# Kernel optimization log

Hardware: AMD Instinct MI355X
Metric: run time of the kernel (lower is better)

## Reference

```python
import jax, jax.numpy as jnp
import numpy as np

N = 20000
E = 640000
D = 128


def setup_inputs() -> dict:
    key = jax.random.key(0)
    ks = jax.random.split(key, 8)
    x = jax.random.normal(ks[0], (N, D), dtype=jnp.float32)
    edge_index = jax.random.randint(ks[1], (2, E), 0, N, dtype=jnp.int64)
    s = 1.0 / np.sqrt(D)
    inp = {"x": x, "edge_index": edge_index}
    for i, layer in enumerate([2, 4, 6]):
        inp[f"W{i+1}"] = jax.random.uniform(ks[layer], (D, D), jnp.float32, -s, s)
        inp[f"b{i+1}"] = jax.random.uniform(ks[layer + 1], (D,), jnp.float32, -s, s)
    return inp


def _gcn_layer(x, src, dst, deg_inv, W, b):
    # linear (torch convention: y = x @ W.T + b), W: [out, in]
    xt = x @ W.T + b
    # gather source-node features, scatter-mean onto targets
    msg = xt[src]                                   # [E, D]
    agg = jax.ops.segment_sum(msg, dst, num_segments=N)  # [N, D]
    agg = agg * deg_inv[:, None]                    # mean over incoming edges
    return jax.nn.relu(agg) + xt


def reference(x, edge_index, W1, b1, W2, b2, W3, b3):
    src, dst = edge_index[0], edge_index[1]
    deg = jax.ops.segment_sum(jnp.ones((E,), jnp.float32), dst, num_segments=N)
    deg_inv = jnp.where(deg > 0, 1.0 / jnp.maximum(deg, 1.0), 0.0)
    for W, b in ((W1, b1), (W2, b2), (W3, b3)):
        x = _gcn_layer(x, src, dst, deg_inv, W, b)
    return x
```

## Files before the change

kernel.cpp:

```cpp
#include <hip/hip_runtime.h>

#define DD 128
#define KC 32
#define MT 64
#define ELLC 128
#define ELLI 124
#define NBMAX 320
#define ACAP 2304
#define AEPW 4096
#define AGGB 2048

__device__ __forceinline__ unsigned f2bf_rne(float f) {
    unsigned u = __float_as_uint(f);
    u += 0x7fffu + ((u >> 16) & 1u);
    return u >> 16;
}

__device__ __forceinline__ void gemm_body(float (*Xs)[MT + 4], float (*Ws)[DD + 4],
                                          const float* x,
                                          const float* __restrict__ W,
                                          const float* __restrict__ b,
                                          float* xt,
                                          unsigned* __restrict__ xtb, int M, int PS, int blk) {
    const int tid  = threadIdx.x;
    const int cg_  = tid & 15;
    const int rg   = tid >> 4;
    const int row0 = blk * MT;

    float acc[4][8];
#pragma unroll
    for (int i = 0; i < 4; ++i)
#pragma unroll
        for (int j = 0; j < 8; ++j) acc[i][j] = 0.0f;

    for (int kc = 0; kc < DD; kc += KC) {
#pragma unroll
        for (int it = 0; it < 2; ++it) {
            int idx = tid + it * 256;
            int r = idx >> 3, kq = idx & 7;
            int gr = row0 + r;
            float4 v = make_float4(0.f, 0.f, 0.f, 0.f);
            if (gr < M) v = *(const float4*)&x[gr * DD + kc + kq * 4];
            Xs[kq * 4 + 0][r] = v.x; Xs[kq * 4 + 1][r] = v.y;
            Xs[kq * 4 + 2][r] = v.z; Xs[kq * 4 + 3][r] = v.w;
        }
#pragma unroll
        for (int it = 0; it < 4; ++it) {
            int idx = tid + it * 256;
            int o = idx >> 3, kq = idx & 7;
            float4 v = *(const float4*)&W[o * DD + kc + kq * 4];
            Ws[kq * 4 + 0][o] = v.x; Ws[kq * 4 + 1][o] = v.y;
            Ws[kq * 4 + 2][o] = v.z; Ws[kq * 4 + 3][o] = v.w;
        }
        __syncthreads();

#pragma unroll 8
        for (int k = 0; k < KC; ++k) {
            float4 xv = *(const float4*)&Xs[k][rg * 4];
            float4 w0 = *(const float4*)&Ws[k][cg_ * 8];
            float4 w1 = *(const float4*)&Ws[k][cg_ * 8 + 4];
            float xr[4] = {xv.x, xv.y, xv.z, xv.w};
            float wc[8] = {w0.x, w0.y, w0.z, w0.w, w1.x, w1.y, w1.z, w1.w};
#pragma unroll
            for (int i = 0; i < 4; ++i)
#pragma unroll
                for (int j = 0; j < 8; ++j) acc[i][j] += xr[i] * wc[j];
        }
        __syncthreads();
    }

    float4 b0 = *(const float4*)&b[cg_ * 8];
    float4 b1 = *(const float4*)&b[cg_ * 8 + 4];
    float bb[8] = {b0.x, b0.y, b0.z, b0.w, b1.x, b1.y, b1.z, b1.w};
#pragma unroll
    for (int i = 0; i < 4; ++i) {
        int gr = row0 + rg * 4 + i;
        if (gr < M) {
            float v[8];
#pragma unroll
            for (int j = 0; j < 8; ++j) v[j] = acc[i][j] + bb[j];
            *(float4*)&xt[gr * DD + cg_ * 8]     = make_float4(v[0], v[1], v[2], v[3]);
            *(float4*)&xt[gr * DD + cg_ * 8 + 4] = make_float4(v[4], v[5], v[6], v[7]);
            uint4 p;
            p.x = f2bf_rne(v[0]) | (f2bf_rne(v[1]) << 16);
            p.y = f2bf_rne(v[2]) | (f2bf_rne(v[3]) << 16);
            p.z = f2bf_rne(v[4]) | (f2bf_rne(v[5]) << 16);
            p.w = f2bf_rne(v[6]) | (f2bf_rne(v[7]) << 16);
            unsigned* xp = xtb + (size_t)(cg_ >> 3) * ((size_t)PS * 32)
                               + (size_t)gr * 32 + ((cg_ & 7) << 2);
            *(uint4*)xp = p;
        }
    }
}

__global__ __launch_bounds__(256) void gemm_xwT(const float* x,
                                                const float* __restrict__ W,
                                                const float* __restrict__ b,
                                                float* xt,
                                                unsigned* __restrict__ xtb, int M, int PS) {
    __shared__ float Xs[KC][MT + 4];
    __shared__ float Ws[KC][DD + 4];
    gemm_body(Xs, Ws, x, W, b, xt, xtb, M, PS, blockIdx.x);
}

__global__ __launch_bounds__(256) void gemm1_plus_binA(const float* x,
                                                       const float* __restrict__ W,
                                                       const float* __restrict__ b,
                                                       float* xt,
                                                       unsigned* __restrict__ xtb, int M, int PS,
                                                       const int* __restrict__ src,
                                                       const int* __restrict__ dst,
                                                       int* __restrict__ bucket_count,
                                                       unsigned* __restrict__ bstore,
                                                       int E, int NB, int PA) {
    __shared__ float Xs[KC][MT + 4];
    __shared__ float Ws[KC][DD + 4];
    __shared__ int hist[NBMAX];
    __shared__ int basec[NBMAX];
    __shared__ int cur[NBMAX];

    if ((int)blockIdx.x >= PA) {
        gemm_body(Xs, Ws, x, W, b, xt, xtb, M, PS, blockIdx.x - PA);
        return;
    }

    const int tid = threadIdx.x;
    for (int i = tid; i < NB; i += 256) hist[i] = 0;
    __syncthreads();

    int dv[16], sv[16];
    const int ebase = blockIdx.x * AEPW;
#pragma unroll
    for (int r = 0; r < 4; ++r) {
        int e = ebase + r * 1024 + tid * 4;
        if (e + 4 <= E) {
            int4 d4 = *(const int4*)&dst[e];
            int4 s4 = *(const int4*)&src[e];
            dv[r*4+0] = d4.x; dv[r*4+1] = d4.y; dv[r*4+2] = d4.z; dv[r*4+3] = d4.w;
            sv[r*4+0] = s4.x; sv[r*4+1] = s4.y; sv[r*4+2] = s4.z; sv[r*4+3] = s4.w;
        } else {
#pragma unroll
            for (int q = 0; q < 4; ++q) {
                int ee = e + q;
                if (ee < E) { dv[r*4+q] = dst[ee]; sv[r*4+q] = src[ee]; }
                else        { dv[r*4+q] = -1;      sv[r*4+q] = 0; }
            }
        }
    }
#pragma unroll
    for (int i = 0; i < 16; ++i)
        if (dv[i] >= 0) atomicAdd(&hist[dv[i] >> 6], 1);
    __syncthreads();

    for (int bk = tid; bk < NB; bk += 256) {
        int h = hist[bk];
        basec[bk] = h ? atomicAdd(&bucket_count[bk], h) : 0;
        cur[bk] = 0;
    }
    __syncthreads();

#pragma unroll
    for (int i = 0; i < 16; ++i) {
        if (dv[i] >= 0) {
            int bk = dv[i] >> 6;
            int pos = basec[bk] + atomicAdd(&cur[bk], 1);
            if (pos < ACAP)
                bstore[bk * ACAP + pos] = ((unsigned)(dv[i] & 63) << 16) | (unsigned)sv[i];
        }
    }
}

__global__ __launch_bounds__(256) void ell_build(const unsigned* __restrict__ bstore,
                                                 const int* __restrict__ bucket_count,
                                                 unsigned short* __restrict__ colell,
                                                 unsigned* __restrict__ xtb,
                                                 int PS, int N) {
    __shared__ int c64[64];
    const int bk = blockIdx.x;
    for (int i = threadIdx.x; i < 64; i += 256) c64[i] = 0;
    __syncthreads();
    int cnt = bucket_count[bk];
    if (cnt > ACAP) cnt = ACAP;
    for (int i = threadIdx.x; i < cnt; i += 256) {
        unsigned code = bstore[bk * ACAP + i];
        int local = (int)(code >> 16);
        int s     = (int)(code & 0xffffu);
        int p = atomicAdd(&c64[local], 1);
        if (p < ELLI)
            colell[((((bk << 6) + local)) << 7) + p] = (unsigned short)s;
    }
    __syncthreads();
    if (threadIdx.x < 64) {
        int node = (bk << 6) + threadIdx.x;
        if (node < N) {
            int d = c64[threadIdx.x];
            int stored = d < ELLI ? d : ELLI;
            int padded = (stored + 3) & ~3;
            unsigned short* row = colell + ((size_t)node << 7);
            for (int p2 = stored; p2 < padded; ++p2) row[p2] = (unsigned short)N;
            row[127] = (unsigned short)(d < 65535 ? d : 65535);
        }
    }
    if (bk == 0 && threadIdx.x >= 64 && threadIdx.x < 80) {
        int i  = threadIdx.x - 64;
        int pl = i >> 3;
        int j  = i & 7;
        *(uint4*)&xtb[((size_t)pl * PS + (size_t)N) * 32 + (size_t)j * 4] =
            make_uint4(0u, 0u, 0u, 0u);
    }
}

__global__ __launch_bounds__(256, 8) void gcn_aggregate(const uint2* __restrict__ xtb2,
                                                        const float* xt,
                                                        const unsigned* __restrict__ colell32,
                                                        float* out, int PS, int N) {
    const int lane = threadIdx.x & 63;
    const int wid  = (int)blockIdx.x * 4 + (threadIdx.x >> 6);
    const int NW   = (int)gridDim.x * 4;
    const int T    = 2 * N;
    if (wid >= T) return;
    const int h = lane & 15;
    const int q = lane >> 4;

    int t = wid;
    int node0 = (t >= N) ? t - N : t;
    unsigned pk = colell32[((size_t)node0 << 6) + lane];

    while (t < T) {
        const int tn    = t + NW;
        const int node  = (t >= N) ? t - N : t;
        const int plane = (t >= N) ? 1 : 0;
        const uint2* __restrict__ xl = xtb2 + (size_t)plane * ((size_t)PS << 4) + h;

        const unsigned w63 = __shfl(pk, 63, 64);
        const int cnt = (int)(w63 >> 16);
        const int cl  = cnt < ELLI ? cnt : ELLI;
        const int cq  = (cl + 3) >> 2;

        float4 t4 = make_float4(0.f, 0.f, 0.f, 0.f);
        if (q == 0)
            t4 = ((const float4*)xt)[(size_t)node * 32 + plane * 16 + h];

        float a0 = 0.f, a1 = 0.f, a2 = 0.f, a3 = 0.f;
        unsigned pkn = 0;
        bool first = true;

        int tq = 0;
        while (tq < cq) {
            int f = cq - tq; if (f > 8) f = 8;
            uint2 u[8];
#pragma unroll
            for (int j = 0; j < 8; ++j) if (j < f) {
                int e = ((tq + j) << 2) | q;
                unsigned w = __shfl(pk, e >> 1, 64);
                int s = (e & 1) ? (int)(w >> 16) : (int)(w & 0xffffu);
                u[j] = xl[(size_t)s << 4];
            }
            if (first) {
                if (tn < T) {
                    int nnode = (tn >= N) ? tn - N : tn;
                    pkn = colell32[((size_t)nnode << 6) + lane];
                }
                first = false;
            }
#pragma unroll
            for (int j = 0; j < 8; ++j) if (j < f) {
                a0 += __uint_as_float(u[j].x << 16);
                a1 += __uint_as_float(u[j].x & 0xffff0000u);
                a2 += __uint_as_float(u[j].y << 16);
                a3 += __uint_as_float(u[j].y & 0xffff0000u);
            }
            tq += f;
        }
        if (first && tn < T) {
            int nnode = (tn >= N) ? tn - N : tn;
            pkn = colell32[((size_t)nnode << 6) + lane];
        }

        a0 += __shfl_down(a0, 32, 64); a1 += __shfl_down(a1, 32, 64);
        a2 += __shfl_down(a2, 32, 64); a3 += __shfl_down(a3, 32, 64);
        a0 += __shfl_down(a0, 16, 64); a1 += __shfl_down(a1, 16, 64);
        a2 += __shfl_down(a2, 16, 64); a3 += __shfl_down(a3, 16, 64);

        if (q == 0) {
            const float di = (cnt > 0) ? (1.0f / (float)cnt) : 0.0f;
            float4 o;
            o.x = fmaxf(a0 * di, 0.f) + t4.x;
            o.y = fmaxf(a1 * di, 0.f) + t4.y;
            o.z = fmaxf(a2 * di, 0.f) + t4.z;
            o.w = fmaxf(a3 * di, 0.f) + t4.w;
            ((float4*)out)[(size_t)node * 32 + plane * 16 + h] = o;
        }

        t = tn;
        pk = pkn;
    }
}

extern "C" void kernel_launch(void* const* d_in, const int* in_sizes, int n_in,
                              void* d_out, int out_size, void* d_ws, size_t ws_size,
                              hipStream_t stream) {
    const float* x  = (const float*)d_in[0];
    const int*   ei = (const int*)d_in[1];
    const float* W1 = (const float*)d_in[2];
    const float* b1 = (const float*)d_in[3];
    const float* W2 = (const float*)d_in[4];
    const float* b2 = (const float*)d_in[5];
    const float* W3 = (const float*)d_in[6];
    const float* b3 = (const float*)d_in[7];

    const int N  = in_sizes[0] / DD;
    const int E  = in_sizes[1] / 2;
    const int PS = N + 1;

    const int* src = ei;
    const int* dst = ei + E;

    const int NB = (N + 63) >> 6;
    const int PA = (E + AEPW - 1) / AEPW;
    const int GB = (N + MT - 1) / MT;

    char* ws = (char*)d_ws;
    size_t off = 0;
    auto alloc = [&](size_t bytes) {
        void* p = ws + off;
        off += (bytes + 255) & ~(size_t)255;
        return p;
    };
    int*            bucket_count = (int*)alloc((size_t)NB * sizeof(int));
    unsigned*       bstore       = (unsigned*)alloc((size_t)NB * ACAP * sizeof(unsigned));
    unsigned short* colell       = (unsigned short*)alloc((size_t)NB * 64 * ELLC * sizeof(unsigned short));
    unsigned*       xtb          = (unsigned*)alloc((size_t)PS * 256);

    float* xbuf = (float*)d_out;

    hipMemsetAsync(bucket_count, 0, (size_t)NB * sizeof(int), stream);
    gemm1_plus_binA<<<PA + GB, 256, 0, stream>>>(x, W1, b1, xbuf, xtb, N, PS,
                                                 src, dst, bucket_count, bstore, E, NB, PA);
    ell_build<<<NB, 256, 0, stream>>>(bstore, bucket_count, colell, xtb, PS, N);

    gcn_aggregate<<<AGGB, 256, 0, stream>>>((const uint2*)xtb, xbuf,
                                            (const unsigned*)colell, xbuf, PS, N);

    gemm_xwT<<<GB, 256, 0, stream>>>(xbuf, W2, b2, xbuf, xtb, N, PS);
    gcn_aggregate<<<AGGB, 256, 0, stream>>>((const uint2*)xtb, xbuf,
                                            (const unsigned*)colell, xbuf, PS, N);

    gemm_xwT<<<GB, 256, 0, stream>>>(xbuf, W3, b3, xbuf, xtb, N, PS);
    gcn_aggregate<<<AGGB, 256, 0, stream>>>((const uint2*)xtb, xbuf,
                                            (const unsigned*)colell, xbuf, PS, N);
}
```

Before: 208.8 us.

## Use split-bf16 MFMA for node linear transforms with precomputed weight splits

```diff
diff --git a/kernel.cpp b/kernel.cpp
--- a/kernel.cpp
+++ b/kernel.cpp
@@ -1,7 +1,6 @@
 #include <hip/hip_runtime.h>
 
 #define DD 128
-#define KC 32
 #define MT 64
 #define ELLC 128
 #define ELLI 124
@@ -10,117 +9,143 @@
 #define AEPW 4096
 #define AGGB 2048
 
+typedef __attribute__((ext_vector_type(8))) short bf16x8;
+typedef __attribute__((ext_vector_type(4))) float f32x4;
+
 __device__ __forceinline__ unsigned f2bf_rne(float f) {
     unsigned u = __float_as_uint(f);
     u += 0x7fffu + ((u >> 16) & 1u);
     return u >> 16;
 }
 
-__device__ __forceinline__ void gemm_body(float (*Xs)[MT + 4], float (*Ws)[DD + 4],
-                                          const float* x,
-                                          const float* __restrict__ W,
-                                          const float* __restrict__ b,
-                                          float* xt,
-                                          unsigned* __restrict__ xtb, int M, int PS, int blk) {
-    const int tid  = threadIdx.x;
-    const int cg_  = tid & 15;
-    const int rg   = tid >> 4;
-    const int row0 = blk * MT;
-
-    float acc[4][8];
-#pragma unroll
-    for (int i = 0; i < 4; ++i)
-#pragma unroll
-        for (int j = 0; j < 8; ++j) acc[i][j] = 0.0f;
-
-    for (int kc = 0; kc < DD; kc += KC) {
-#pragma unroll
-        for (int it = 0; it < 2; ++it) {
-            int idx = tid + it * 256;
-            int r = idx >> 3, kq = idx & 7;
-            int gr = row0 + r;
-            float4 v = make_float4(0.f, 0.f, 0.f, 0.f);
-            if (gr < M) v = *(const float4*)&x[gr * DD + kc + kq * 4];
-            Xs[kq * 4 + 0][r] = v.x; Xs[kq * 4 + 1][r] = v.y;
-            Xs[kq * 4 + 2][r] = v.z; Xs[kq * 4 + 3][r] = v.w;
-        }
-#pragma unroll
-        for (int it = 0; it < 4; ++it) {
-            int idx = tid + it * 256;
-            int o = idx >> 3, kq = idx & 7;
-            float4 v = *(const float4*)&W[o * DD + kc + kq * 4];
-            Ws[kq * 4 + 0][o] = v.x; Ws[kq * 4 + 1][o] = v.y;
-            Ws[kq * 4 + 2][o] = v.z; Ws[kq * 4 + 3][o] = v.w;
-        }
-        __syncthreads();
-
-#pragma unroll 8
-        for (int k = 0; k < KC; ++k) {
-            float4 xv = *(const float4*)&Xs[k][rg * 4];
-            float4 w0 = *(const float4*)&Ws[k][cg_ * 8];
-            float4 w1 = *(const float4*)&Ws[k][cg_ * 8 + 4];
-            float xr[4] = {xv.x, xv.y, xv.z, xv.w};
-            float wc[8] = {w0.x, w0.y, w0.z, w0.w, w1.x, w1.y, w1.z, w1.w};
-#pragma unroll
-            for (int i = 0; i < 4; ++i)
-#pragma unroll
-                for (int j = 0; j < 8; ++j) acc[i][j] += xr[i] * wc[j];
-        }
-        __syncthreads();
-    }
-
-    float4 b0 = *(const float4*)&b[cg_ * 8];
-    float4 b1 = *(const float4*)&b[cg_ * 8 + 4];
-    float bb[8] = {b0.x, b0.y, b0.z, b0.w, b1.x, b1.y, b1.z, b1.w};
-#pragma unroll
-    for (int i = 0; i < 4; ++i) {
-        int gr = row0 + rg * 4 + i;
+__device__ __forceinline__ bf16x8 pack8(const unsigned h[8]) {
+    union { uint4 u; bf16x8 v; } t;
+    t.u.x = h[0] | (h[1] << 16);
+    t.u.y = h[2] | (h[3] << 16);
+    t.u.z = h[4] | (h[5] << 16);
+    t.u.w = h[6] | (h[7] << 16);
+    return t.v;
+}
+
+__global__ __launch_bounds__(256) void prep(const float* __restrict__ W1,
+                                            const float* __restrict__ W2,
+                                            const float* __restrict__ W3,
+                                            unsigned short* __restrict__ whi,
+                                            unsigned short* __restrict__ wlo,
+                                            int* __restrict__ bucket_count, int NB) {
+    const int bk = blockIdx.x;
+    if (bk < 3) {
+        const float* W = (bk == 0) ? W1 : (bk == 1 ? W2 : W3);
+        unsigned short* h = whi + bk * (DD * DD);
+        unsigned short* l = wlo + bk * (DD * DD);
+        for (int i = threadIdx.x; i < DD * DD; i += 256) {
+            float x = W[i];
+            unsigned uh = f2bf_rne(x);
+            float fh = __uint_as_float(uh << 16);
+            h[i] = (unsigned short)uh;
+            l[i] = (unsigned short)f2bf_rne(x - fh);
+        }
+    } else {
+        for (int i = threadIdx.x; i < NB; i += 256) bucket_count[i] = 0;
+    }
+}
+
+__device__ __forceinline__ void gemm_body_mfma(const float* x,
+                                               const unsigned short* __restrict__ whi,
+                                               const unsigned short* __restrict__ wlo,
+                                               const float* __restrict__ b,
+                                               float* xt,
+                                               unsigned short* __restrict__ xtb16,
+                                               int M, int PS, int blk) {
+    const int lane = threadIdx.x & 63;
+    const int wv   = threadIdx.x >> 6;
+    const int r0   = blk * MT + wv * 16;
+    const int m    = lane & 15;
+    const int kg   = lane >> 4;
+    const int gr   = r0 + m;
+
+    f32x4 acc[8];
+#pragma unroll
+    for (int c = 0; c < 8; ++c) acc[c] = (f32x4){0.f, 0.f, 0.f, 0.f};
+
+#pragma unroll
+    for (int ks = 0; ks < 4; ++ks) {
+        const int kb = ks * 32 + kg * 8;
+        float4 v0 = make_float4(0.f, 0.f, 0.f, 0.f), v1 = v0;
         if (gr < M) {
-            float v[8];
-#pragma unroll
-            for (int j = 0; j < 8; ++j) v[j] = acc[i][j] + bb[j];
-            *(float4*)&xt[gr * DD + cg_ * 8]     = make_float4(v[0], v[1], v[2], v[3]);
-            *(float4*)&xt[gr * DD + cg_ * 8 + 4] = make_float4(v[4], v[5], v[6], v[7]);
-            uint4 p;
-            p.x = f2bf_rne(v[0]) | (f2bf_rne(v[1]) << 16);
-            p.y = f2bf_rne(v[2]) | (f2bf_rne(v[3]) << 16);
-            p.z = f2bf_rne(v[4]) | (f2bf_rne(v[5]) << 16);
-            p.w = f2bf_rne(v[6]) | (f2bf_rne(v[7]) << 16);
-            unsigned* xp = xtb + (size_t)(cg_ >> 3) * ((size_t)PS * 32)
-                               + (size_t)gr * 32 + ((cg_ & 7) << 2);
-            *(uint4*)xp = p;
+            v0 = *(const float4*)&x[(size_t)gr * DD + kb];
+            v1 = *(const float4*)&x[(size_t)gr * DD + kb + 4];
+        }
+        float xv[8] = {v0.x, v0.y, v0.z, v0.w, v1.x, v1.y, v1.z, v1.w};
+        unsigned hh[8], ll[8];
+#pragma unroll
+        for (int j = 0; j < 8; ++j) {
+            unsigned uh = f2bf_rne(xv[j]);
+            float fh = __uint_as_float(uh << 16);
+            hh[j] = uh;
+            ll[j] = f2bf_rne(xv[j] - fh);
+        }
+        bf16x8 ah = pack8(hh), al = pack8(ll);
+
+#pragma unroll
+        for (int c = 0; c < 8; ++c) {
+            const int ncol = c * 16 + m;
+            union { uint4 u; bf16x8 v; } bh, bl;
+            bh.u = *(const uint4*)&whi[(size_t)ncol * DD + kb];
+            bl.u = *(const uint4*)&wlo[(size_t)ncol * DD + kb];
+            acc[c] = __builtin_amdgcn_mfma_f32_16x16x32_bf16(ah, bh.v, acc[c], 0, 0, 0);
+            acc[c] = __builtin_amdgcn_mfma_f32_16x16x32_bf16(ah, bl.v, acc[c], 0, 0, 0);
+            acc[c] = __builtin_amdgcn_mfma_f32_16x16x32_bf16(al, bh.v, acc[c], 0, 0, 0);
+        }
+    }
+
+    const int rbase = r0 + kg * 4;
+#pragma unroll
+    for (int c = 0; c < 8; ++c) {
+        const int ncol  = c * 16 + m;
+        const float bias = b[ncol];
+        const int plane = ncol >> 6;
+        const int c64   = ncol & 63;
+#pragma unroll
+        for (int rg = 0; rg < 4; ++rg) {
+            const int grr = rbase + rg;
+            if (grr < M) {
+                float v = acc[c][rg] + bias;
+                xt[(size_t)grr * DD + ncol] = v;
+                xtb16[((size_t)plane * PS + grr) * 64 + c64] = (unsigned short)f2bf_rne(v);
+            }
         }
     }
 }
 
 __global__ __launch_bounds__(256) void gemm_xwT(const float* x,
-                                                const float* __restrict__ W,
+                                                const unsigned short* __restrict__ whi,
+                                                const unsigned short* __restrict__ wlo,
                                                 const float* __restrict__ b,
                                                 float* xt,
-                                                unsigned* __restrict__ xtb, int M, int PS) {
-    __shared__ float Xs[KC][MT + 4];
-    __shared__ float Ws[KC][DD + 4];
-    gemm_body(Xs, Ws, x, W, b, xt, xtb, M, PS, blockIdx.x);
+                                                unsigned short* __restrict__ xtb16,
+                                                int M, int PS) {
+    gemm_body_mfma(x, whi, wlo, b, xt, xtb16, M, PS, blockIdx.x);
 }
 
 __global__ __launch_bounds__(256) void gemm1_plus_binA(const float* x,
-                                                       const float* __restrict__ W,
+                                                       const unsigned short* __restrict__ whi,
+                                                       const unsigned short* __restrict__ wlo,
                                                        const float* __restrict__ b,
                                                        float* xt,
-                                                       unsigned* __restrict__ xtb, int M, int PS,
+                                                       unsigned short* __restrict__ xtb16,
+                                                       int M, int PS,
                                                        const int* __restrict__ src,
                                                        const int* __restrict__ dst,
                                                        int* __restrict__ bucket_count,
                                                        unsigned* __restrict__ bstore,
                                                        int E, int NB, int PA) {
-    __shared__ float Xs[KC][MT + 4];
-    __shared__ float Ws[KC][DD + 4];
     __shared__ int hist[NBMAX];
     __shared__ int basec[NBMAX];
     __shared__ int cur[NBMAX];
 
     if ((int)blockIdx.x >= PA) {
-        gemm_body(Xs, Ws, x, W, b, xt, xtb, M, PS, blockIdx.x - PA);
+        gemm_body_mfma(x, whi, wlo, b, xt, xtb16, M, PS, blockIdx.x - PA);
         return;
     }
 
@@ -331,22 +356,28 @@
     unsigned*       bstore       = (unsigned*)alloc((size_t)NB * ACAP * sizeof(unsigned));
     unsigned short* colell       = (unsigned short*)alloc((size_t)NB * 64 * ELLC * sizeof(unsigned short));
     unsigned*       xtb          = (unsigned*)alloc((size_t)PS * 256);
+    unsigned short* whi          = (unsigned short*)alloc((size_t)3 * DD * DD * sizeof(unsigned short));
+    unsigned short* wlo          = (unsigned short*)alloc((size_t)3 * DD * DD * sizeof(unsigned short));
 
     float* xbuf = (float*)d_out;
-
-    hipMemsetAsync(bucket_count, 0, (size_t)NB * sizeof(int), stream);
-    gemm1_plus_binA<<<PA + GB, 256, 0, stream>>>(x, W1, b1, xbuf, xtb, N, PS,
+    unsigned short* xtb16 = (unsigned short*)xtb;
+
+    prep<<<4, 256, 0, stream>>>(W1, W2, W3, whi, wlo, bucket_count, NB);
+
+    gemm1_plus_binA<<<PA + GB, 256, 0, stream>>>(x, whi, wlo, b1, xbuf, xtb16, N, PS,
                                                  src, dst, bucket_count, bstore, E, NB, PA);
     ell_build<<<NB, 256, 0, stream>>>(bstore, bucket_count, colell, xtb, PS, N);
 
     gcn_aggregate<<<AGGB, 256, 0, stream>>>((const uint2*)xtb, xbuf,
                                             (const unsigned*)colell, xbuf, PS, N);
 
-    gemm_xwT<<<GB, 256, 0, stream>>>(xbuf, W2, b2, xbuf, xtb, N, PS);
+    gemm_xwT<<<GB, 256, 0, stream>>>(xbuf, whi + DD * DD, wlo + DD * DD, b2,
+                                     xbuf, xtb16, N, PS);
     gcn_aggregate<<<AGGB, 256, 0, stream>>>((const uint2*)xtb, xbuf,
                                             (const unsigned*)colell, xbuf, PS, N);
 
-    gemm_xwT<<<GB, 256, 0, stream>>>(xbuf, W3, b3, xbuf, xtb, N, PS);
+    gemm_xwT<<<GB, 256, 0, stream>>>(xbuf, whi + 2 * DD * DD, wlo + 2 * DD * DD, b3,
+                                     xbuf, xtb16, N, PS);
     gcn_aggregate<<<AGGB, 256, 0, stream>>>((const uint2*)xtb, xbuf,
                                             (const unsigned*)colell, xbuf, PS, N);
 }
```

After: 226.0 us. 1.08x slower.

## Build ELL adjacency by direct per-node atomic scatter instead of bucketed two-pass

Applied to the files above, without the earlier changes.

```diff
diff --git a/kernel.cpp b/kernel.cpp
--- a/kernel.cpp
+++ b/kernel.cpp
@@ -5,8 +5,6 @@
 #define MT 64
 #define ELLC 128
 #define ELLI 124
-#define NBMAX 320
-#define ACAP 2304
 #define AEPW 4096
 #define AGGB 2048
 
@@ -103,31 +101,25 @@
     gemm_body(Xs, Ws, x, W, b, xt, xtb, M, PS, blockIdx.x);
 }
 
-__global__ __launch_bounds__(256) void gemm1_plus_binA(const float* x,
+__global__ __launch_bounds__(256) void gemm1_plus_scat(const float* x,
                                                        const float* __restrict__ W,
                                                        const float* __restrict__ b,
                                                        float* xt,
                                                        unsigned* __restrict__ xtb, int M, int PS,
                                                        const int* __restrict__ src,
                                                        const int* __restrict__ dst,
-                                                       int* __restrict__ bucket_count,
-                                                       unsigned* __restrict__ bstore,
-                                                       int E, int NB, int PA) {
+                                                       int* __restrict__ deg,
+                                                       unsigned short* __restrict__ colell,
+                                                       int E, int SB) {
     __shared__ float Xs[KC][MT + 4];
     __shared__ float Ws[KC][DD + 4];
-    __shared__ int hist[NBMAX];
-    __shared__ int basec[NBMAX];
-    __shared__ int cur[NBMAX];
-
-    if ((int)blockIdx.x >= PA) {
-        gemm_body(Xs, Ws, x, W, b, xt, xtb, M, PS, blockIdx.x - PA);
+
+    if ((int)blockIdx.x >= SB) {
+        gemm_body(Xs, Ws, x, W, b, xt, xtb, M, PS, blockIdx.x - SB);
         return;
     }
 
     const int tid = threadIdx.x;
-    for (int i = tid; i < NB; i += 256) hist[i] = 0;
-    __syncthreads();
-
     int dv[16], sv[16];
     const int ebase = blockIdx.x * AEPW;
 #pragma unroll
@@ -148,61 +140,30 @@
         }
     }
 #pragma unroll
-    for (int i = 0; i < 16; ++i)
-        if (dv[i] >= 0) atomicAdd(&hist[dv[i] >> 6], 1);
-    __syncthreads();
-
-    for (int bk = tid; bk < NB; bk += 256) {
-        int h = hist[bk];
-        basec[bk] = h ? atomicAdd(&bucket_count[bk], h) : 0;
-        cur[bk] = 0;
-    }
-    __syncthreads();
-
-#pragma unroll
     for (int i = 0; i < 16; ++i) {
         if (dv[i] >= 0) {
-            int bk = dv[i] >> 6;
-            int pos = basec[bk] + atomicAdd(&cur[bk], 1);
-            if (pos < ACAP)
-                bstore[bk * ACAP + pos] = ((unsigned)(dv[i] & 63) << 16) | (unsigned)sv[i];
-        }
-    }
-}
-
-__global__ __launch_bounds__(256) void ell_build(const unsigned* __restrict__ bstore,
-                                                 const int* __restrict__ bucket_count,
-                                                 unsigned short* __restrict__ colell,
-                                                 unsigned* __restrict__ xtb,
-                                                 int PS, int N) {
-    __shared__ int c64[64];
-    const int bk = blockIdx.x;
-    for (int i = threadIdx.x; i < 64; i += 256) c64[i] = 0;
-    __syncthreads();
-    int cnt = bucket_count[bk];
-    if (cnt > ACAP) cnt = ACAP;
-    for (int i = threadIdx.x; i < cnt; i += 256) {
-        unsigned code = bstore[bk * ACAP + i];
-        int local = (int)(code >> 16);
-        int s     = (int)(code & 0xffffu);
-        int p = atomicAdd(&c64[local], 1);
-        if (p < ELLI)
-            colell[((((bk << 6) + local)) << 7) + p] = (unsigned short)s;
-    }
-    __syncthreads();
-    if (threadIdx.x < 64) {
-        int node = (bk << 6) + threadIdx.x;
-        if (node < N) {
-            int d = c64[threadIdx.x];
-            int stored = d < ELLI ? d : ELLI;
-            int padded = (stored + 3) & ~3;
-            unsigned short* row = colell + ((size_t)node << 7);
-            for (int p2 = stored; p2 < padded; ++p2) row[p2] = (unsigned short)N;
-            row[127] = (unsigned short)(d < 65535 ? d : 65535);
-        }
-    }
-    if (bk == 0 && threadIdx.x >= 64 && threadIdx.x < 80) {
-        int i  = threadIdx.x - 64;
+            int pos = atomicAdd(&deg[dv[i]], 1);
+            if (pos < ELLI)
+                colell[((size_t)dv[i] << 7) + pos] = (unsigned short)sv[i];
+        }
+    }
+}
+
+__global__ __launch_bounds__(256) void ell_pad(unsigned short* __restrict__ colell,
+                                               const int* __restrict__ deg,
+                                               unsigned* __restrict__ xtb,
+                                               int PS, int N) {
+    const int node = (int)blockIdx.x * 256 + threadIdx.x;
+    if (node < N) {
+        int d = deg[node];
+        int stored = d < ELLI ? d : ELLI;
+        int padded = (stored + 3) & ~3;
+        unsigned short* row = colell + ((size_t)node << 7);
+        for (int p2 = stored; p2 < padded; ++p2) row[p2] = (unsigned short)N;
+        row[127] = (unsigned short)(d < 65535 ? d : 65535);
+    }
+    if (blockIdx.x == 0 && threadIdx.x < 16) {
+        int i  = threadIdx.x;
         int pl = i >> 3;
         int j  = i & 7;
         *(uint4*)&xtb[((size_t)pl * PS + (size_t)N) * 32 + (size_t)j * 4] =
@@ -316,9 +277,9 @@
     const int* src = ei;
     const int* dst = ei + E;
 
-    const int NB = (N + 63) >> 6;
-    const int PA = (E + AEPW - 1) / AEPW;
+    const int SB = (E + AEPW - 1) / AEPW;
     const int GB = (N + MT - 1) / MT;
+    const int PB = (N + 255) / 256;
 
     char* ws = (char*)d_ws;
     size_t off = 0;
@@ -327,17 +288,16 @@
         off += (bytes + 255) & ~(size_t)255;
         return p;
     };
-    int*            bucket_count = (int*)alloc((size_t)NB * sizeof(int));
-    unsigned*       bstore       = (unsigned*)alloc((size_t)NB * ACAP * sizeof(unsigned));
-    unsigned short* colell       = (unsigned short*)alloc((size_t)NB * 64 * ELLC * sizeof(unsigned short));
-    unsigned*       xtb          = (unsigned*)alloc((size_t)PS * 256);
+    int*            deg    = (int*)alloc((size_t)N * sizeof(int));
+    unsigned short* colell = (unsigned short*)alloc((size_t)N * ELLC * sizeof(unsigned short));
+    unsigned*       xtb    = (unsigned*)alloc((size_t)PS * 256);
 
     float* xbuf = (float*)d_out;
 
-    hipMemsetAsync(bucket_count, 0, (size_t)NB * sizeof(int), stream);
-    gemm1_plus_binA<<<PA + GB, 256, 0, stream>>>(x, W1, b1, xbuf, xtb, N, PS,
-                                                 src, dst, bucket_count, bstore, E, NB, PA);
-    ell_build<<<NB, 256, 0, stream>>>(bstore, bucket_count, colell, xtb, PS, N);
+    hipMemsetAsync(deg, 0, (size_t)N * sizeof(int), stream);
+    gemm1_plus_scat<<<SB + GB, 256, 0, stream>>>(x, W1, b1, xbuf, xtb, N, PS,
+                                                 src, dst, deg, colell, E, SB);
+    ell_pad<<<PB, 256, 0, stream>>>(colell, deg, xtb, PS, N);
 
     gcn_aggregate<<<AGGB, 256, 0, stream>>>((const uint2*)xtb, xbuf,
                                             (const unsigned*)colell, xbuf, PS, N);
```

Result: slower. 217.7 us (+4.2%).
